# Kernel optimization log

Hardware: AMD Instinct MI355X
Metric: run time of the kernel (lower is better)

The kernel has to match this reference:

```python
import jax, jax.numpy as jnp
import numpy as np

B, P, N = 2, 8192, 24
C1, C2 = 32, 32
K, A = 13, 12  # kernel points (12 anchors + center), rotation anchors


def _icosahedron_vs():
    phi = (1.0 + np.sqrt(5.0)) / 2.0
    v = []
    for s1 in (1.0, -1.0):
        for s2 in (1.0, -1.0):
            v.append([0.0, s1, s2 * phi])
            v.append([s1, s2 * phi, 0.0])
            v.append([s2 * phi, 0.0, s1])
    v = np.array(v, dtype=np.float32)
    return v / np.linalg.norm(v, axis=1, keepdims=True)


def setup_inputs() -> dict:
    key = jax.random.key(0)
    ks = jax.random.split(key, 6)
    rng = np.random.RandomState(0)
    vertices = jax.random.normal(ks[0], (B, P, 3), jnp.float32)
    neighbor_index = jax.random.randint(ks[1], (B, P, N), 0, P)
    feature_map = jax.random.normal(ks[2], (B, C1, K, P, A), jnp.float32)
    W = jax.random.normal(ks[3], (C2, C1, 36), jnp.float32) * 0.05
    bias = jax.random.normal(ks[4], (C2, 5), jnp.float32) * 0.05
    k_pos_w = jax.random.normal(ks[5], (C2, 36), jnp.float32) * 0.1
    vs = jnp.asarray(_icosahedron_vs())
    # precomputed rotation-group trace index buffers (valid-range stand-ins for
    # the fr.get_relativeV_index / idx_map precomputation in the original repo)
    idx_map = jnp.asarray(rng.randint(0, 36, size=(K * A,)), jnp.int32)          # [156] -> 36 classes
    trace_idxv_rot = jnp.asarray(np.stack([rng.permutation(K) for _ in range(A)]), jnp.int32)  # [A(r), K]
    trace_idx_rot = jnp.asarray(np.stack([rng.permutation(A) for _ in range(A)]), jnp.int32)   # [A(r), A]
    lvl = jnp.asarray(np.concatenate([rng.randint(0, 4, size=(A,)), np.array([4])]), jnp.int32)  # [K] shell level per kernel point
    return dict(neighbor_index=neighbor_index, vertices=vertices, feature_map=feature_map,
                W=W, bias=bias, k_pos_w=k_pos_w, vs=vs, idx_map=idx_map,
                trace_idxv_rot=trace_idxv_rot, trace_idx_rot=trace_idx_rot, lvl=lvl)


def reference(neighbor_index, vertices, feature_map, W, bias, k_pos_w, vs,
              idx_map, trace_idxv_rot, trace_idx_rot, lvl):
    c2, c1, _ = W.shape
    # unit-normalized neighbor directions: [b, p, n, 3]
    nbr = jax.vmap(lambda v, i: v[i])(vertices, neighbor_index)
    d = nbr - vertices[:, :, None, :]
    ndn = d / jnp.maximum(jnp.linalg.norm(d, axis=-1, keepdims=True), 1e-12)
    # expand the 36 equivariance classes to the full (k, a) kernel grid
    k_pos_w_ori = k_pos_w[:, idx_map].reshape(c2, K, A)        # [d, k, a]
    W_re = W[:, :, idx_map].reshape(c2, c1, K, A)              # [d, c, k, a]
    # rotate kernel-point and anchor axes per output rotation r (gather by trace idx)
    Ik = trace_idxv_rot[:, :, None]   # [r, k, 1], values in [0, K)
    Ia = trace_idx_rot[:, None, :]    # [r, 1, a], values in [0, A)
    W_eff = jnp.transpose(W_re[:, :, Ik, Ia], (0, 1, 3, 4, 2))   # [d, c, k, a, r]
    k_eff = jnp.transpose(k_pos_w_ori[:, Ik, Ia], (0, 2, 3, 1))  # [d, k, a, r]
    # learned kernel-point positions on S2 and positional weights vs local geometry
    k_pos_ori = jnp.einsum('dka,ac->dkc', k_pos_w_ori, vs)
    k_pos_ori = k_pos_ori / jnp.maximum(jnp.linalg.norm(k_pos_ori, axis=-1, keepdims=True), 1e-12)
    mean_dir = ndn.mean(axis=2)                                  # [b, p, 3]
    pw = jax.nn.relu(jnp.einsum('bpc,dkc->bdpk', mean_dir, k_pos_ori))
    # equivariant conv: small per-point matmul over (c, a) per kernel point, then k-weighted sum
    WT = W_eff * k_eff[:, None]                                  # [d, c, k, a, r]
    agg = jnp.einsum('dckar,bckpa->bdkpr', WT, feature_map)
    out = jnp.einsum('bdkpr,bdpk->bdpr', agg, pw)
    bias_eff = bias[:, lvl][:, trace_idxv_rot].sum(axis=-1)      # [d, r]
    return jax.nn.relu(out + bias_eff[None, :, None, :])
```

## Files before the change

### kernel.cpp

```cpp
#include <hip/hip_runtime.h>
#include <cstdint>
#include <cstddef>

#define B_   2
#define P_   8192
#define NN_  24
#define C1_  32
#define C2_  32
#define K_   13
#define A_   12
#define DR_  384
#define CA_  384
#define PT_  32
#define BPAD 408

typedef __attribute__((ext_vector_type(8))) short short8;
typedef __attribute__((ext_vector_type(4))) float floatx4;

__device__ __forceinline__ unsigned short f2bf(float f) {
    union { float f; unsigned int u; } v; v.f = f;
    unsigned int u = v.u;
    return (unsigned short)((u + 0x7fffu + ((u >> 16) & 1u)) >> 16);
}


__global__ void build_wt(const float* __restrict__ W, const float* __restrict__ kpw,
                         const int* __restrict__ idx_map, const int* __restrict__ tivr,
                         const int* __restrict__ tir, unsigned short* __restrict__ WT2) {
    int id = blockIdx.x * 256 + threadIdx.x;
    const int TOT = K_ * DR_ * CA_;
    if (id >= TOT) return;
    int ca = id % CA_;
    int t1 = id / CA_;
    int dr = t1 % DR_;
    int k  = t1 / DR_;
    int d = dr / 12, r = dr % 12;
    int c = ca / 12, a = ca % 12;
    int kk = tivr[r * K_ + k];
    int ia = tir[r * A_ + a];
    int m  = idx_map[kk * A_ + ia];
    WT2[id] = f2bf(W[(d * C1_ + c) * 36 + m] * kpw[d * 36 + m]);
}

__global__ void build_md(const int* __restrict__ nbr, const float* __restrict__ verts,
                         float* __restrict__ md) {
    int t = blockIdx.x * 256 + threadIdx.x;
    if (t >= B_ * P_) return;
    const float* vp = verts + (size_t)t * 3;
    float vx = vp[0], vy = vp[1], vz = vp[2];
    int b = t / P_;
    const int* np = nbr + (size_t)t * NN_;
    float ax = 0.f, ay = 0.f, az = 0.f;
    for (int n = 0; n < NN_; n++) {
        int j = np[n];
        const float* vq = verts + ((size_t)b * P_ + j) * 3;
        float dx = vq[0] - vx, dy = vq[1] - vy, dz = vq[2] - vz;
        float nn = sqrtf(dx * dx + dy * dy + dz * dz);
        float inv = 1.f / fmaxf(nn, 1e-12f);
        ax += dx * inv; ay += dy * inv; az += dz * inv;
    }
    const float s = 1.f / 24.f;
    md[t * 3 + 0] = ax * s; md[t * 3 + 1] = ay * s; md[t * 3 + 2] = az * s;
}

__global__ void build_kpo(const float* __restrict__ kpw, const int* __restrict__ idx_map,
                          const float* __restrict__ vs, float* __restrict__ kpo) {
    int t = blockIdx.x * 64 + threadIdx.x;
    if (t >= C2_ * K_) return;
    int d = t / K_, k = t % K_;
    float x = 0.f, y = 0.f, z = 0.f;
    for (int a = 0; a < A_; a++) {
        float w = kpw[d * 36 + idx_map[k * A_ + a]];
        x += w * vs[a * 3 + 0]; y += w * vs[a * 3 + 1]; z += w * vs[a * 3 + 2];
    }
    float nn = sqrtf(x * x + y * y + z * z);
    float inv = 1.f / fmaxf(nn, 1e-12f);
    kpo[t * 3 + 0] = x * inv; kpo[t * 3 + 1] = y * inv; kpo[t * 3 + 2] = z * inv;
}

__global__ void build_be(const float* __restrict__ bias, const int* __restrict__ lvl,
                         const int* __restrict__ tivr, float* __restrict__ be) {
    int t = blockIdx.x * 64 + threadIdx.x;
    if (t >= DR_) return;
    int d = t / 12, r = t % 12;
    float s = 0.f;
    for (int k = 0; k < K_; k++) s += bias[d * 5 + lvl[tivr[r * K_ + k]]];
    be[t] = s;
}

__global__ __launch_bounds__(256, 2) void main_gemm(
    const float* __restrict__ fm, const unsigned short* __restrict__ WT,
    const float* __restrict__ md, const float* __restrict__ kpo,
    const float* __restrict__ be, float* __restrict__ out) {

    __shared__ __attribute__((aligned(16))) unsigned short Bs[2][PT_][BPAD];
    __shared__ float pwS[2][C2_][PT_ + 1];
    __shared__ float mdS[PT_][3];
    __shared__ float kpoS[C2_ * K_ * 3];
    __shared__ float biasS[DR_];

    const int tid  = threadIdx.x;
    const int bid  = blockIdx.x;
    const int b    = bid >> 8;
    const int p0   = (bid & 255) << 5;
    const int lane = tid & 63;
    const int wid  = tid >> 6;
    const int rowm = lane & 15;
    const int quad = lane >> 4;

    floatx4 pf[12];
    int pf_c[12], pf_jj[12];
    #pragma unroll
    for (int j = 0; j < 12; j++) {
        int f = j * 256 + tid;
        pf_c[j]  = f / 96;
        pf_jj[j] = f - pf_c[j] * 96;
    }

    #define LOAD_PF(kk)                                                                  \
        { _Pragma("unroll")                                                              \
          for (int j = 0; j < 12; j++) {                                                 \
            const floatx4* src = (const floatx4*)(fm +                                   \
                ((((size_t)b * C1_ + pf_c[j]) * K_ + (kk)) * P_ + p0) * A_) + pf_jj[j];  \
            pf[j] = __builtin_nontemporal_load(src);                                     \
          } }

    #define STORE_PF(bufw)                                                               \
        { _Pragma("unroll")                                                              \
          for (int j = 0; j < 12; j++) {                                                 \
            int pl = pf_jj[j] / 3, aseg = (pf_jj[j] - pl * 3) * 4;                       \
            ushort4 pk = make_ushort4(f2bf(pf[j][0]), f2bf(pf[j][1]),                    \
                                      f2bf(pf[j][2]), f2bf(pf[j][3]));                   \
            *(ushort4*)&Bs[bufw][pl][pf_c[j] * A_ + aseg] = pk;                          \
          } }

    #define CALC_PW(bufw, kk)                                                            \
        { for (int i = tid; i < C2_ * PT_; i += 256) {                                   \
            int d = i >> 5, pl = i & 31;                                                 \
            const float* kv = &kpoS[(d * K_ + (kk)) * 3];                                \
            float s = mdS[pl][0] * kv[0] + mdS[pl][1] * kv[1] + mdS[pl][2] * kv[2];      \
            pwS[bufw][d][pl] = fmaxf(s, 0.f);                                            \
          } }

    const unsigned short* awbase = WT + (size_t)(wid * 96 + rowm) * CA_ + quad * 8;
    #define LOAD_A(dst, kk, ch)                                                          \
        { const unsigned short* ap = awbase + (size_t)(kk) * (DR_ * CA_) + (ch) * 32;    \
          _Pragma("unroll")                                                              \
          for (int mt = 0; mt < 6; mt++) dst[mt] = *(const short8*)(ap + mt * 16 * CA_); }

    for (int i = tid; i < PT_ * 3; i += 256) {
        int p = i / 3, c = i % 3;
        mdS[p][c] = md[((size_t)b * P_ + p0 + p) * 3 + c];
    }
    for (int i = tid; i < C2_ * K_ * 3; i += 256) kpoS[i] = kpo[i];
    for (int i = tid; i < DR_; i += 256) biasS[i] = be[i];

    floatx4 acc_o[6][2];
    floatx4 acc_k[6][2];
    #pragma unroll
    for (int mt = 0; mt < 6; mt++)
        #pragma unroll
        for (int nt = 0; nt < 2; nt++) { acc_o[mt][nt] = (floatx4)0.f; acc_k[mt][nt] = (floatx4)0.f; }

    short8 abuf[3][6];

    LOAD_PF(0);
    __syncthreads();
    LOAD_A(abuf[0], 0, 0);
    LOAD_A(abuf[1], 0, 1);
    STORE_PF(0);
    CALC_PW(0, 0);
    LOAD_PF(1);

    for (int k = 0; k < K_; k++) {
        const int buf = k & 1;
        __syncthreads();

        #pragma unroll
        for (int ch = 0; ch < 12; ch++) {
            if (ch < 10) LOAD_A(abuf[(ch + 2) % 3], k, ch + 2);
            short8 bfr[2];
            #pragma unroll
            for (int nt = 0; nt < 2; nt++)
                bfr[nt] = *(const short8*)(&Bs[buf][nt * 16 + rowm][ch * 32 + quad * 8]);
            const short8* af = abuf[ch % 3];
            #pragma unroll
            for (int mt = 0; mt < 6; mt++)
                #pragma unroll
                for (int nt = 0; nt < 2; nt++)
                    acc_k[mt][nt] = __builtin_amdgcn_mfma_f32_16x16x32_bf16(af[mt], bfr[nt], acc_k[mt][nt], 0, 0, 0);
        }

        #pragma unroll
        for (int mt = 0; mt < 6; mt++) {
            const int drb = wid * 96 + mt * 16 + quad * 4;
            const int d = drb / 12;
            #pragma unroll
            for (int nt = 0; nt < 2; nt++) {
                const float pv = pwS[buf][d][nt * 16 + rowm];
                #pragma unroll
                for (int reg = 0; reg < 4; reg++) {
                    acc_o[mt][nt][reg] += pv * acc_k[mt][nt][reg];
                    acc_k[mt][nt][reg] = 0.f;
                }
            }
        }

        if (k + 1 < K_) {
            LOAD_A(abuf[0], k + 1, 0);
            LOAD_A(abuf[1], k + 1, 1);
            STORE_PF(buf ^ 1);
            CALC_PW(buf ^ 1, k + 1);
        }
        if (k + 2 < K_) LOAD_PF(k + 2);
    }

    #pragma unroll
    for (int mt = 0; mt < 6; mt++) {
        const int drb = wid * 96 + mt * 16 + quad * 4;
        const int d = drb / 12, r0 = drb - d * 12;
        floatx4 bz;
        #pragma unroll
        for (int reg = 0; reg < 4; reg++) bz[reg] = biasS[drb + reg];
        #pragma unroll
        for (int nt = 0; nt < 2; nt++) {
            const int p = p0 + nt * 16 + rowm;
            floatx4 v = acc_o[mt][nt] + bz;
            #pragma unroll
            for (int reg = 0; reg < 4; reg++) v[reg] = fmaxf(v[reg], 0.f);
            __builtin_nontemporal_store(v,
                (floatx4*)(out + ((((size_t)b * C2_ + d) * P_ + p) * A_ + r0)));
        }
    }
}

extern "C" void kernel_launch(void* const* d_in, const int* in_sizes, int n_in,
                              void* d_out, int out_size, void* d_ws, size_t ws_size,
                              hipStream_t stream) {
    const int*   nbr     = (const int*)d_in[0];
    const float* verts   = (const float*)d_in[1];
    const float* fm      = (const float*)d_in[2];
    const float* W       = (const float*)d_in[3];
    const float* bias    = (const float*)d_in[4];
    const float* kpw     = (const float*)d_in[5];
    const float* vs      = (const float*)d_in[6];
    const int*   idx_map = (const int*)d_in[7];
    const int*   tivr    = (const int*)d_in[8];
    const int*   tir     = (const int*)d_in[9];
    const int*   lvl     = (const int*)d_in[10];
    float* out = (float*)d_out;

    char* ws = (char*)d_ws;
    unsigned short* WT2 = (unsigned short*)ws;
    float* md_ws  = (float*)(ws + 4000000);
    float* kpo_ws = (float*)(ws + 4200000);
    float* be_ws  = (float*)(ws + 4210000);

    {
        const int TOT = K_ * DR_ * CA_;
        build_wt<<<(TOT + 255) / 256, 256, 0, stream>>>(W, kpw, idx_map, tivr, tir, WT2);
    }
    build_md<<<(B_ * P_) / 256, 256, 0, stream>>>(nbr, verts, md_ws);
    build_kpo<<<7, 64, 0, stream>>>(kpw, idx_map, vs, kpo_ws);
    build_be<<<6, 64, 0, stream>>>(bias, lvl, tivr, be_ws);

    main_gemm<<<B_ * (P_ / PT_), 256, 0, stream>>>(fm, WT2, md_ws, kpo_ws, be_ws, out);
}
```

Baseline: 748.6 us.

## Double point tile to 64 with 512-thread blocks and restructure prefetch schedule

Each block now covers 64 points with 8 waves, and each wave handles 48 output rows across 4 point sub-tiles. This halves the number of times the bf16 weight matrix is streamed from memory per point. The staging of the next k-slice (bf16 conversion and positional weights) moves to the start of the iteration, and the global feature prefetch is split across the MFMA chunks so loads overlap compute. Nontemporal loads and stores become plain ones. The larger shared-memory footprint (Bs doubles to about 104KB) may reduce occupancy or exceed the LDS limit needed for two blocks per CU.

Result: faster. 605.9 us (-19.1%).

```diff
diff --git a/kernel.cpp b/kernel.cpp
--- a/kernel.cpp
+++ b/kernel.cpp
@@ -11,7 +11,7 @@
 #define A_   12
 #define DR_  384
 #define CA_  384
-#define PT_  32
+#define PT_  64
 #define BPAD 408
 
 typedef __attribute__((ext_vector_type(8))) short short8;
@@ -88,7 +88,7 @@
     be[t] = s;
 }
 
-__global__ __launch_bounds__(256, 2) void main_gemm(
+__global__ __launch_bounds__(512, 2) void main_gemm(
     const float* __restrict__ fm, const unsigned short* __restrict__ WT,
     const float* __restrict__ md, const float* __restrict__ kpo,
     const float* __restrict__ be, float* __restrict__ out) {
@@ -101,8 +101,8 @@
 
     const int tid  = threadIdx.x;
     const int bid  = blockIdx.x;
-    const int b    = bid >> 8;
-    const int p0   = (bid & 255) << 5;
+    const int b    = bid >> 7;
+    const int p0   = (bid & 127) << 6;
     const int lane = tid & 63;
     const int wid  = tid >> 6;
     const int rowm = lane & 15;
@@ -112,57 +112,61 @@
     int pf_c[12], pf_jj[12];
     #pragma unroll
     for (int j = 0; j < 12; j++) {
-        int f = j * 256 + tid;
-        pf_c[j]  = f / 96;
-        pf_jj[j] = f - pf_c[j] * 96;
-    }
-
-    #define LOAD_PF(kk)                                                                  \
-        { _Pragma("unroll")                                                              \
-          for (int j = 0; j < 12; j++) {                                                 \
+        int f = j * 512 + tid;
+        pf_c[j]  = f / 192;
+        pf_jj[j] = f - pf_c[j] * 192;
+    }
+
+    #define LOAD_PF_PART(kk, j0, j1)                                                     \
+        do { _Pragma("unroll")                                                           \
+          for (int j = (j0); j < (j1); j++) {                                            \
             const floatx4* src = (const floatx4*)(fm +                                   \
                 ((((size_t)b * C1_ + pf_c[j]) * K_ + (kk)) * P_ + p0) * A_) + pf_jj[j];  \
-            pf[j] = __builtin_nontemporal_load(src);                                     \
-          } }
+            pf[j] = *src;                                                                \
+          } } while (0)
+    #define LOAD_PF(kk) LOAD_PF_PART(kk, 0, 12)
 
     #define STORE_PF(bufw)                                                               \
-        { _Pragma("unroll")                                                              \
+        do { _Pragma("unroll")                                                           \
           for (int j = 0; j < 12; j++) {                                                 \
             int pl = pf_jj[j] / 3, aseg = (pf_jj[j] - pl * 3) * 4;                       \
             ushort4 pk = make_ushort4(f2bf(pf[j][0]), f2bf(pf[j][1]),                    \
                                       f2bf(pf[j][2]), f2bf(pf[j][3]));                   \
             *(ushort4*)&Bs[bufw][pl][pf_c[j] * A_ + aseg] = pk;                          \
-          } }
+          } } while (0)
 
     #define CALC_PW(bufw, kk)                                                            \
-        { for (int i = tid; i < C2_ * PT_; i += 256) {                                   \
-            int d = i >> 5, pl = i & 31;                                                 \
+        do { _Pragma("unroll")                                                           \
+          for (int it = 0; it < 4; it++) {                                               \
+            int i = it * 512 + tid;                                                      \
+            int d = i >> 6, pl = i & 63;                                                 \
             const float* kv = &kpoS[(d * K_ + (kk)) * 3];                                \
             float s = mdS[pl][0] * kv[0] + mdS[pl][1] * kv[1] + mdS[pl][2] * kv[2];      \
             pwS[bufw][d][pl] = fmaxf(s, 0.f);                                            \
-          } }
-
-    const unsigned short* awbase = WT + (size_t)(wid * 96 + rowm) * CA_ + quad * 8;
+          } } while (0)
+
+    const unsigned short* awbase = WT + (size_t)(wid * 48 + rowm) * CA_ + quad * 8;
     #define LOAD_A(dst, kk, ch)                                                          \
-        { const unsigned short* ap = awbase + (size_t)(kk) * (DR_ * CA_) + (ch) * 32;    \
+        do { const unsigned short* ap = awbase + (size_t)(kk) * (DR_ * CA_) + (ch) * 32; \
           _Pragma("unroll")                                                              \
-          for (int mt = 0; mt < 6; mt++) dst[mt] = *(const short8*)(ap + mt * 16 * CA_); }
-
-    for (int i = tid; i < PT_ * 3; i += 256) {
+          for (int mt = 0; mt < 3; mt++) dst[mt] = *(const short8*)(ap + mt * 16 * CA_); \
+        } while (0)
+
+    for (int i = tid; i < PT_ * 3; i += 512) {
         int p = i / 3, c = i % 3;
         mdS[p][c] = md[((size_t)b * P_ + p0 + p) * 3 + c];
     }
-    for (int i = tid; i < C2_ * K_ * 3; i += 256) kpoS[i] = kpo[i];
-    for (int i = tid; i < DR_; i += 256) biasS[i] = be[i];
-
-    floatx4 acc_o[6][2];
-    floatx4 acc_k[6][2];
+    for (int i = tid; i < C2_ * K_ * 3; i += 512) kpoS[i] = kpo[i];
+    for (int i = tid; i < DR_; i += 512) biasS[i] = be[i];
+
+    floatx4 acc_o[3][4];
+    floatx4 acc_k[3][4];
     #pragma unroll
-    for (int mt = 0; mt < 6; mt++)
-        #pragma unroll
-        for (int nt = 0; nt < 2; nt++) { acc_o[mt][nt] = (floatx4)0.f; acc_k[mt][nt] = (floatx4)0.f; }
-
-    short8 abuf[3][6];
+    for (int mt = 0; mt < 3; mt++)
+        #pragma unroll
+        for (int nt = 0; nt < 4; nt++) { acc_o[mt][nt] = (floatx4)0.f; acc_k[mt][nt] = (floatx4)0.f; }
+
+    short8 abuf[3][3];
 
     LOAD_PF(0);
     __syncthreads();
@@ -176,27 +180,41 @@
         const int buf = k & 1;
         __syncthreads();
 
+        if (k + 1 < K_) {
+            STORE_PF(buf ^ 1);
+            CALC_PW(buf ^ 1, k + 1);
+        }
+
         #pragma unroll
         for (int ch = 0; ch < 12; ch++) {
-            if (ch < 10) LOAD_A(abuf[(ch + 2) % 3], k, ch + 2);
-            short8 bfr[2];
-            #pragma unroll
-            for (int nt = 0; nt < 2; nt++)
+            if (ch < 10) {
+                LOAD_A(abuf[(ch + 2) % 3], k, ch + 2);
+            } else if (k + 1 < K_) {
+                LOAD_A(abuf[(ch + 2) % 3], k + 1, ch - 10);
+            }
+            if (k + 2 < K_) {
+                if (ch == 6)      { LOAD_PF_PART(k + 2, 0, 4); }
+                else if (ch == 7) { LOAD_PF_PART(k + 2, 4, 8); }
+                else if (ch == 8) { LOAD_PF_PART(k + 2, 8, 12); }
+            }
+            short8 bfr[4];
+            #pragma unroll
+            for (int nt = 0; nt < 4; nt++)
                 bfr[nt] = *(const short8*)(&Bs[buf][nt * 16 + rowm][ch * 32 + quad * 8]);
             const short8* af = abuf[ch % 3];
             #pragma unroll
-            for (int mt = 0; mt < 6; mt++)
+            for (int mt = 0; mt < 3; mt++)
                 #pragma unroll
-                for (int nt = 0; nt < 2; nt++)
+                for (int nt = 0; nt < 4; nt++)
                     acc_k[mt][nt] = __builtin_amdgcn_mfma_f32_16x16x32_bf16(af[mt], bfr[nt], acc_k[mt][nt], 0, 0, 0);
         }
 
         #pragma unroll
-        for (int mt = 0; mt < 6; mt++) {
-            const int drb = wid * 96 + mt * 16 + quad * 4;
+        for (int mt = 0; mt < 3; mt++) {
+            const int drb = wid * 48 + mt * 16 + quad * 4;
             const int d = drb / 12;
             #pragma unroll
-            for (int nt = 0; nt < 2; nt++) {
+            for (int nt = 0; nt < 4; nt++) {
                 const float pv = pwS[buf][d][nt * 16 + rowm];
                 #pragma unroll
                 for (int reg = 0; reg < 4; reg++) {
@@ -205,31 +223,22 @@
                 }
             }
         }
-
-        if (k + 1 < K_) {
-            LOAD_A(abuf[0], k + 1, 0);
-            LOAD_A(abuf[1], k + 1, 1);
-            STORE_PF(buf ^ 1);
-            CALC_PW(buf ^ 1, k + 1);
-        }
-        if (k + 2 < K_) LOAD_PF(k + 2);
     }
 
     #pragma unroll
-    for (int mt = 0; mt < 6; mt++) {
-        const int drb = wid * 96 + mt * 16 + quad * 4;
+    for (int mt = 0; mt < 3; mt++) {
+        const int drb = wid * 48 + mt * 16 + quad * 4;
         const int d = drb / 12, r0 = drb - d * 12;
         floatx4 bz;
         #pragma unroll
         for (int reg = 0; reg < 4; reg++) bz[reg] = biasS[drb + reg];
         #pragma unroll
-        for (int nt = 0; nt < 2; nt++) {
+        for (int nt = 0; nt < 4; nt++) {
             const int p = p0 + nt * 16 + rowm;
             floatx4 v = acc_o[mt][nt] + bz;
             #pragma unroll
             for (int reg = 0; reg < 4; reg++) v[reg] = fmaxf(v[reg], 0.f);
-            __builtin_nontemporal_store(v,
-                (floatx4*)(out + ((((size_t)b * C2_ + d) * P_ + p) * A_ + r0)));
+            *(floatx4*)(out + ((((size_t)b * C2_ + d) * P_ + p) * A_ + r0)) = v;
         }
     }
 }
@@ -264,5 +273,5 @@
     build_kpo<<<7, 64, 0, stream>>>(kpw, idx_map, vs, kpo_ws);
     build_be<<<6, 64, 0, stream>>>(bias, lvl, tivr, be_ws);
 
-    main_gemm<<<B_ * (P_ / PT_), 256, 0, stream>>>(fm, WT2, md_ws, kpo_ws, be_ws, out);
-}
+    main_gemm<<<B_ * (P_ / PT_), 512, 0, stream>>>(fm, WT2, md_ws, kpo_ws, be_ws, out);
+}
```
